# Optimization experiments

Hardware: AMD Instinct MI355X
Metric: run time of the kernel (lower is better)

The kernel has to match this reference:

```python
import jax, jax.numpy as jnp
import numpy as np

SEQ, BATCH, EMB, HID = 512, 256, 256, 512


def setup_inputs() -> dict:
    key = jax.random.key(0)
    ks = jax.random.split(key, 6)
    s_x = 1.0 / np.sqrt(EMB)
    s_h = 1.0 / np.sqrt(HID)
    return {
        "X": jax.random.normal(ks[0], (SEQ, BATCH, EMB), dtype=jnp.float32),
        # torch Linear weights are [out_features, in_features]
        "Wfx": jax.random.normal(ks[1], (HID, EMB), dtype=jnp.float32) * s_x,
        "Wix": jax.random.normal(ks[2], (HID, EMB), dtype=jnp.float32) * s_x,
        "Wox": jax.random.normal(ks[3], (HID, EMB), dtype=jnp.float32) * s_x,
        "Wax": jax.random.normal(ks[4], (HID, EMB), dtype=jnp.float32) * s_x,
        "Waa": jax.random.normal(ks[5], (HID, HID), dtype=jnp.float32) * s_h,
        # module initializes all biases to ones
        "bf": jnp.ones((HID,), dtype=jnp.float32),
        "bi": jnp.ones((HID,), dtype=jnp.float32),
        "bo": jnp.ones((HID,), dtype=jnp.float32),
        "ba": jnp.ones((HID,), dtype=jnp.float32),
    }


def reference(X, Wfx, Wix, Wox, Wax, Waa, bf, bi, bo, ba):
    # X: [seq, batch, emb]. Returns final hidden state h: [batch, hidden].
    batch = X.shape[1]
    hid = Waa.shape[0]

    def step(carry, x):
        h, c = carry
        ah = h @ Waa.T  # shared across all gates, as in the original
        # NOTE: original adds the bias twice (b + ... + b), kept faithfully
        ft = jax.nn.sigmoid(x @ Wfx.T + ah + 2.0 * bf)
        it = jax.nn.sigmoid(x @ Wix.T + ah + 2.0 * bi)
        ot = jax.nn.sigmoid(x @ Wox.T + ah + 2.0 * bo)
        cp = jnp.tanh(x @ Wax.T + ah + ba)
        c = ft * c + it * cp
        h = ot * jnp.tanh(c)
        return (h, c), None

    h0 = jnp.zeros((batch, hid), dtype=X.dtype)
    (h, _c), _ = jax.lax.scan(step, (h0, h0), X)
    return h
```

## Files before the change

### kernel.cpp

```cpp
#include <hip/hip_runtime.h>

#define SEQL 512
#define BATCH 256
#define EMB 256
#define HID 512
#define NTOT 2048

typedef __attribute__((ext_vector_type(8))) short bf16x8;
typedef __attribute__((ext_vector_type(4))) float f32x4;
typedef unsigned short u16;

static __device__ __forceinline__ u16 f2bf(float f) {
  unsigned u = __float_as_uint(f);
  u += 0x7FFFu + ((u >> 16) & 1u);
  return (u16)(u >> 16);
}
static __device__ __forceinline__ float bf2f(u16 s) {
  return __uint_as_float(((unsigned)s) << 16);
}
static __device__ __forceinline__ float sigmoidf_(float z) {
  return 1.f / (1.f + __expf(-z));
}
static __device__ __forceinline__ float tanhf_(float x) {
  float e = __expf(2.f * fabsf(x));
  float t = 1.f - 2.f / (e + 1.f);
  return copysignf(t, x);
}
static __device__ __forceinline__ f32x4 mfma16(bf16x8 a, bf16x8 b, f32x4 c) {
  return __builtin_amdgcn_mfma_f32_16x16x32_bf16(a, b, c, 0, 0, 0);
}
static __device__ __forceinline__ void gld16(const u16* g, u16* l) {
  __builtin_amdgcn_global_load_lds((const __attribute__((address_space(1))) void*)g,
                                   (__attribute__((address_space(3))) void*)l, 16, 0, 0);
}
static __device__ __forceinline__ bf16x8 ldx4_dev(const u16* p) {
  bf16x8 r;
  asm volatile("global_load_dwordx4 %0, %1, off sc1" : "=v"(r) : "v"(p));
  return r;
}
static __device__ __forceinline__ void st2_dev(u16* p, unsigned v) {
  asm volatile("global_store_short %0, %1, off sc1" :: "v"(p), "v"(v) : "memory");
}

__global__ void k_split(const float* __restrict__ src, u16* __restrict__ hi,
                        u16* __restrict__ lo, int n) {
  for (int i = blockIdx.x * blockDim.x + threadIdx.x; i < n;
       i += gridDim.x * blockDim.x) {
    float v = src[i];
    u16 h = f2bf(v);
    hi[i] = h;
    lo[i] = f2bf(v - bf2f(h));
  }
}

__global__ void k_bias2(const float* __restrict__ bf_, const float* __restrict__ bi_,
                        const float* __restrict__ bo_, const float* __restrict__ ba_,
                        float* __restrict__ bias2) {
  int n = blockIdx.x * blockDim.x + threadIdx.x;
  if (n >= NTOT) return;
  int g = n >> 9, j = n & 511;
  const float* p = (g == 0) ? bf_ : (g == 1) ? bi_ : (g == 2) ? bo_ : ba_;
  bias2[n] = ((g < 3) ? 2.f : 1.f) * p[j];
}

__global__ __launch_bounds__(256) void k_gemm(
    const u16* __restrict__ Ahi, const u16* __restrict__ Alo,
    const u16* __restrict__ Bhi, const u16* __restrict__ Blo,
    const float* __restrict__ bias2, float* __restrict__ G2) {
  __shared__ u16 lds[4][128 * 64];
  const int tid = threadIdx.x;
  const int lane = tid & 63;
  const int w = tid >> 6;
  const int wm = (w >> 1) * 64, wn = (w & 1) * 64;
  const int m0 = blockIdx.y * 128, n0 = blockIdx.x * 128;
  const int l15 = lane & 15, lhi = lane >> 4;

  f32x4 acc[4][4] = {};

  for (int k0 = 0; k0 < EMB; k0 += 64) {
    __syncthreads();
    for (int c = 0; c < 4; ++c) {
      int idx = tid + c * 256;
      int row = idx >> 3;
      int col = (idx & 7) * 8;
      long ga = (long)(m0 + row) * EMB + k0 + col;
      long gb = (long)(n0 + row) * EMB + k0 + col;
      gld16(Ahi + ga, &lds[0][idx * 8]);
      gld16(Alo + ga, &lds[1][idx * 8]);
      gld16(Bhi + gb, &lds[2][idx * 8]);
      gld16(Blo + gb, &lds[3][idx * 8]);
    }
    __syncthreads();
#pragma unroll
    for (int ks = 0; ks < 2; ++ks) {
      int ko = ks * 32 + lhi * 8;
      bf16x8 ah[4], al[4], bh[4], bl[4];
#pragma unroll
      for (int f = 0; f < 4; ++f) {
        int ra = (wm + f * 16 + l15) * 64 + ko;
        int rb = (wn + f * 16 + l15) * 64 + ko;
        ah[f] = *(const bf16x8*)&lds[0][ra];
        al[f] = *(const bf16x8*)&lds[1][ra];
        bh[f] = *(const bf16x8*)&lds[2][rb];
        bl[f] = *(const bf16x8*)&lds[3][rb];
      }
#pragma unroll
      for (int i = 0; i < 4; ++i)
#pragma unroll
        for (int j = 0; j < 4; ++j) {
          acc[i][j] = mfma16(ah[i], bh[j], acc[i][j]);
          acc[i][j] = mfma16(ah[i], bl[j], acc[i][j]);
          acc[i][j] = mfma16(al[i], bh[j], acc[i][j]);
        }
    }
  }
#pragma unroll
  for (int j = 0; j < 4; ++j) {
    int n = n0 + wn + j * 16 + l15;
    float bv = bias2[n];
    int g = n >> 9, jj = n & 511;
    int j16 = jj >> 4, j15 = jj & 15;
#pragma unroll
    for (int i = 0; i < 4; ++i) {
      int mb = m0 + wm + i * 16 + lhi * 4;
      int tloc = mb >> 8, brow = mb & 255;
      int bgrp = brow >> 4, bq = (brow >> 2) & 3;
      f32x4 v = acc[i][j];
      v[0] += bv; v[1] += bv; v[2] += bv; v[3] += bv;
      size_t addr = ((((size_t)(tloc * 16 + bgrp) * 32 + j16) * 4 + g) * 4 + bq) * 64 +
                    (size_t)j15 * 4;
      *(f32x4*)&G2[addr] = v;
    }
  }
}

__global__ __launch_bounds__(256, 1) void k_rnn(
    const u16* __restrict__ WaaHi, const u16* __restrict__ WaaLo,
    const float* __restrict__ G2,
    u16* __restrict__ h0hi, u16* __restrict__ h0lo,
    u16* __restrict__ h1hi, u16* __restrict__ h1lo,
    float* __restrict__ cSave, unsigned* __restrict__ flags,
    float* __restrict__ out, int t0, int nsteps) {
  const int tid = threadIdx.x;
  const int lane = tid & 63;
  const int w = tid >> 6;
  const int jsub = w >> 1, ksub = w & 1;
  const int l15 = lane & 15, lhi = lane >> 4;
  const int bid = blockIdx.x;
  const int grp = ((bid & 7) << 1) | ((bid >> 3) & 1);
  const int mem = bid >> 4;
  const int b0 = grp * 16;
  const int j0 = mem * 32 + jsub * 16;
  const int j16 = mem * 2 + jsub;
  const bool owner = (ksub == 0);

  __shared__ float red[2][64][4];

  bf16x8 wh[8], wl[8];
  {
    long base = (long)(j0 + l15) * HID + ksub * 256 + lhi * 8;
#pragma unroll
    for (int s = 0; s < 8; ++s) {
      wh[s] = *(const bf16x8*)&WaaHi[base + s * 32];
      wl[s] = *(const bf16x8*)&WaaLo[base + s * 32];
    }
#pragma unroll
    for (int s = 0; s < 8; ++s) {
      asm volatile("" : "+v"(wh[s]));
      asm volatile("" : "+v"(wl[s]));
    }
  }

  f32x4 c = {0.f, 0.f, 0.f, 0.f};
  const long cbase = (long)(b0 + lhi * 4) * HID + j0 + l15;
  if (owner && t0 > 0) {
#pragma unroll
    for (int r = 0; r < 4; ++r) c[r] = cSave[cbase + (long)r * HID];
  }

  const long abase = (long)(b0 + l15) * HID + ksub * 256 + lhi * 8;
  unsigned* flag = &flags[grp * 32];

  float gv[4][4];
  if (owner) {
    size_t tb = ((size_t)(0 * 16 + grp) * 32 + j16) * 1024;
#pragma unroll
    for (int g = 0; g < 4; ++g) {
      f32x4 v = *(const f32x4*)&G2[tb + (size_t)(g * 4 + lhi) * 64 + (size_t)l15 * 4];
#pragma unroll
      for (int r = 0; r < 4; ++r) gv[g][r] = v[r];
    }
  }

  for (int tl = 0; tl < nsteps; ++tl) {
    const int gt = t0 + tl;
    const u16* hHi = (gt & 1) ? h1hi : h0hi;
    const u16* hLo = (gt & 1) ? h1lo : h0lo;
    u16* nHi = (gt & 1) ? h0hi : h1hi;
    u16* nLo = (gt & 1) ? h0lo : h1lo;

    bf16x8 ah[8], al[8];
#pragma unroll
    for (int s = 0; s < 8; ++s) {
      ah[s] = ldx4_dev(hHi + abase + s * 32);
      al[s] = ldx4_dev(hLo + abase + s * 32);
    }
    asm volatile("s_waitcnt vmcnt(0)" ::: "memory");
    __builtin_amdgcn_sched_barrier(0);

    f32x4 a0 = {0.f, 0.f, 0.f, 0.f}, a1 = a0, a2 = a0;
#pragma unroll
    for (int s = 0; s < 8; ++s) {
      a0 = mfma16(ah[s], wh[s], a0);
      a1 = mfma16(ah[s], wl[s], a1);
      a2 = mfma16(al[s], wh[s], a2);
    }
    f32x4 acc = (a0 + a1) + a2;

    if (ksub == 1) *(f32x4*)&red[jsub][lane][0] = acc;

    float gvn[4][4];
    if (owner && tl + 1 < nsteps) {
      size_t tb = ((size_t)((tl + 1) * 16 + grp) * 32 + j16) * 1024;
#pragma unroll
      for (int g = 0; g < 4; ++g) {
        f32x4 v = *(const f32x4*)&G2[tb + (size_t)(g * 4 + lhi) * 64 + (size_t)l15 * 4];
#pragma unroll
        for (int r = 0; r < 4; ++r) gvn[g][r] = v[r];
      }
    }

    __syncthreads();
    if (owner) {
      f32x4 p = *(const f32x4*)&red[jsub][lane][0];
      acc += p;
#pragma unroll
      for (int r = 0; r < 4; ++r) {
        float z = acc[r];
        float ft = sigmoidf_(gv[0][r] + z);
        float it = sigmoidf_(gv[1][r] + z);
        float ot = sigmoidf_(gv[2][r] + z);
        float cp = tanhf_(gv[3][r] + z);
        c[r] = ft * c[r] + it * cp;
        float h = ot * tanhf_(c[r]);
        int b = b0 + lhi * 4 + r;
        int jj = j0 + l15;
        if (gt == SEQL - 1) {
          out[(long)b * HID + jj] = h;
        } else {
          u16 hh = f2bf(h);
          st2_dev(&nHi[(long)b * HID + jj], (unsigned)hh);
          st2_dev(&nLo[(long)b * HID + jj], (unsigned)f2bf(h - bf2f(hh)));
        }
      }
      if (tl + 1 < nsteps) {
#pragma unroll
        for (int g = 0; g < 4; ++g)
#pragma unroll
          for (int r = 0; r < 4; ++r) gv[g][r] = gvn[g][r];
      }
    }

    if (tl + 1 < nsteps) {
      asm volatile("s_waitcnt vmcnt(0)" ::: "memory");
      if ((tid & 127) == 0) {
        unsigned one = 1u;
        asm volatile("global_atomic_add %0, %1, off sc1" :: "v"(flag), "v"(one)
                     : "memory");
      }
      if (tid == 0) {
        unsigned tgt = 32u * (unsigned)(tl + 1);
        long guard = 0;
        unsigned v;
        for (;;) {
          asm volatile("global_load_dword %0, %1, off sc0 sc1\n\ts_waitcnt vmcnt(0)"
                       : "=v"(v) : "v"(flag) : "memory");
          if (v >= tgt) break;
          __builtin_amdgcn_s_sleep(1);
          if (++guard > (1L << 22)) break;
        }
      }
      __syncthreads();
    }
  }

  if (owner && t0 + nsteps < SEQL) {
#pragma unroll
    for (int r = 0; r < 4; ++r) cSave[cbase + (long)r * HID] = c[r];
  }
}

extern "C" void kernel_launch(void* const* d_in, const int* in_sizes, int n_in,
                              void* d_out, int out_size, void* d_ws, size_t ws_size,
                              hipStream_t stream) {
  const float* X   = (const float*)d_in[0];
  const float* Wfx = (const float*)d_in[1];
  const float* Wix = (const float*)d_in[2];
  const float* Wox = (const float*)d_in[3];
  const float* Wax = (const float*)d_in[4];
  const float* Waa = (const float*)d_in[5];
  const float* bfp = (const float*)d_in[6];
  const float* bip = (const float*)d_in[7];
  const float* bop = (const float*)d_in[8];
  const float* bap = (const float*)d_in[9];
  float* out = (float*)d_out;

  char* ws = (char*)d_ws;
  size_t off = 0;
  auto take = [&](size_t n) {
    void* p = ws + off;
    off += (n + 255) & ~(size_t)255;
    return p;
  };
  u16* WxHi  = (u16*)take((size_t)NTOT * EMB * 2);
  u16* WxLo  = (u16*)take((size_t)NTOT * EMB * 2);
  u16* WaaHi = (u16*)take((size_t)HID * HID * 2);
  u16* WaaLo = (u16*)take((size_t)HID * HID * 2);
  float* bias2 = (float*)take((size_t)NTOT * 4);
  u16* h0hi = (u16*)take((size_t)BATCH * HID * 2);
  u16* h0lo = (u16*)take((size_t)BATCH * HID * 2);
  u16* h1hi = (u16*)take((size_t)BATCH * HID * 2);
  u16* h1lo = (u16*)take((size_t)BATCH * HID * 2);
  float* cSave = (float*)take((size_t)BATCH * HID * 4);
  unsigned* flags = (unsigned*)take(16 * 32 * 4);
  size_t fixed_end = off;

  const size_t perstep = (size_t)BATCH * EMB * 2 * 2 + (size_t)BATCH * NTOT * 4;
  int C = 0;
  const int cands[] = {512, 256, 128, 64, 32, 16, 8, 4, 2, 1};
  for (int cand : cands)
    if (fixed_end + (size_t)cand * perstep <= ws_size) { C = cand; break; }
  if (C == 0) return;

  u16* XcHi = (u16*)take((size_t)C * BATCH * EMB * 2);
  u16* XcLo = (u16*)take((size_t)C * BATCH * EMB * 2);
  float* G2 = (float*)take((size_t)C * BATCH * NTOT * 4);

  const float* wx[4] = {Wfx, Wix, Wox, Wax};
  for (int g = 0; g < 4; ++g)
    k_split<<<256, 256, 0, stream>>>(wx[g], WxHi + (size_t)g * HID * EMB,
                                     WxLo + (size_t)g * HID * EMB, HID * EMB);
  k_split<<<512, 256, 0, stream>>>(Waa, WaaHi, WaaLo, HID * HID);
  k_bias2<<<8, 256, 0, stream>>>(bfp, bip, bop, bap, bias2);
  hipMemsetAsync(h0hi, 0, (size_t)BATCH * HID * 2 * 2, stream);

  const int nch = SEQL / C;
  for (int ch = 0; ch < nch; ++ch) {
    int t0 = ch * C;
    hipMemsetAsync(flags, 0, 16 * 32 * 4, stream);
    k_split<<<2048, 256, 0, stream>>>(X + (size_t)t0 * BATCH * EMB, XcHi, XcLo,
                                      C * BATCH * EMB);
    dim3 gg(NTOT / 128, C * 2);
    k_gemm<<<gg, 256, 0, stream>>>(XcHi, XcLo, WxHi, WxLo, bias2, G2);
    k_rnn<<<256, 256, 0, stream>>>(WaaHi, WaaLo, G2, h0hi, h0lo, h1hi, h1lo,
                                   cSave, flags, out, t0, C);
  }
}
```

Measured before the change: 3.807 ms.

## Restructure recurrent kernel to 64 blocks with LDS-resident weights and fused X split

The recurrent kernel now runs on 64 blocks instead of 256, and each block owns 128 hidden units. Waa is pre-packed into MFMA fragment order: the hi half stays in registers and the lo half is staged in LDS. The aim is fewer blocks taking part in each per-step cross-block barrier, and larger per-wave work. The X hi/lo split is fused into the input GEMM's LDS staging, which removes a separate split kernel and its buffers. The G2 layout is changed to match the new tiling. The trade-off is that per-step compute per block grows about fourfold and runs on only 64 CUs, so the serial step latency could rise.

After: 4.966 ms. 1.3x slower.

```diff
diff --git a/kernel.cpp b/kernel.cpp
--- a/kernel.cpp
+++ b/kernel.cpp
@@ -8,6 +8,7 @@
 
 typedef __attribute__((ext_vector_type(8))) short bf16x8;
 typedef __attribute__((ext_vector_type(4))) float f32x4;
+typedef __attribute__((ext_vector_type(4))) unsigned short us4;
 typedef unsigned short u16;
 
 static __device__ __forceinline__ u16 f2bf(float f) {
@@ -40,6 +41,16 @@
 }
 static __device__ __forceinline__ void st2_dev(u16* p, unsigned v) {
   asm volatile("global_store_short %0, %1, off sc1" :: "v"(p), "v"(v) : "memory");
+}
+static __device__ __forceinline__ void flag_add_dev(unsigned* p) {
+  unsigned one = 1u;
+  asm volatile("global_atomic_add %0, %1, off sc1" :: "v"(p), "v"(one) : "memory");
+}
+static __device__ __forceinline__ unsigned flag_poll_dev(const unsigned* p) {
+  unsigned v;
+  asm volatile("global_load_dword %0, %1, off sc0 sc1\ns_waitcnt vmcnt(0)"
+               : "=v"(v) : "v"(p) : "memory");
+  return v;
 }
 
 __global__ void k_split(const float* __restrict__ src, u16* __restrict__ hi,
@@ -63,8 +74,27 @@
   bias2[n] = ((g < 3) ? 2.f : 1.f) * p[j];
 }
 
+__global__ void k_packW(const float* __restrict__ Waa, u16* __restrict__ WPhi,
+                        u16* __restrict__ WPlo) {
+  int idx = blockIdx.x * 256 + threadIdx.x;
+  int lane = idx & 63;
+  int fi = idx >> 6;
+  if (fi >= 512) return;
+  int kf = fi & 7, nf = (fi >> 3) & 3, w = (fi >> 5) & 3, mem = fi >> 7;
+  int j = mem * 128 + (w >> 1) * 64 + nf * 16 + (lane & 15);
+  int k0 = (w & 1) * 256 + kf * 32 + (lane >> 4) * 8;
+  size_t base = (size_t)idx * 8;
+#pragma unroll
+  for (int e = 0; e < 8; ++e) {
+    float v = Waa[(size_t)j * HID + k0 + e];
+    u16 h = f2bf(v);
+    WPhi[base + e] = h;
+    WPlo[base + e] = f2bf(v - bf2f(h));
+  }
+}
+
 __global__ __launch_bounds__(256) void k_gemm(
-    const u16* __restrict__ Ahi, const u16* __restrict__ Alo,
+    const float* __restrict__ X,
     const u16* __restrict__ Bhi, const u16* __restrict__ Blo,
     const float* __restrict__ bias2, float* __restrict__ G2) {
   __shared__ u16 lds[4][128 * 64];
@@ -79,16 +109,30 @@
 
   for (int k0 = 0; k0 < EMB; k0 += 64) {
     __syncthreads();
+#pragma unroll
     for (int c = 0; c < 4; ++c) {
       int idx = tid + c * 256;
       int row = idx >> 3;
       int col = (idx & 7) * 8;
-      long ga = (long)(m0 + row) * EMB + k0 + col;
-      long gb = (long)(n0 + row) * EMB + k0 + col;
-      gld16(Ahi + ga, &lds[0][idx * 8]);
-      gld16(Alo + ga, &lds[1][idx * 8]);
+      size_t gb = (size_t)(n0 + row) * EMB + k0 + col;
       gld16(Bhi + gb, &lds[2][idx * 8]);
       gld16(Blo + gb, &lds[3][idx * 8]);
+    }
+#pragma unroll
+    for (int c = 0; c < 8; ++c) {
+      int idx = tid + c * 256;
+      int row = idx >> 4;
+      int c4 = (idx & 15) * 4;
+      f32x4 xv = *(const f32x4*)&X[(size_t)(m0 + row) * EMB + k0 + c4];
+      us4 h4, l4;
+#pragma unroll
+      for (int e = 0; e < 4; ++e) {
+        u16 h = f2bf(xv[e]);
+        h4[e] = h;
+        l4[e] = f2bf(xv[e] - bf2f(h));
+      }
+      *(us4*)&lds[0][row * 64 + c4] = h4;
+      *(us4*)&lds[1][row * 64 + c4] = l4;
     }
     __syncthreads();
 #pragma unroll
@@ -119,174 +163,161 @@
     int n = n0 + wn + j * 16 + l15;
     float bv = bias2[n];
     int g = n >> 9, jj = n & 511;
-    int j16 = jj >> 4, j15 = jj & 15;
 #pragma unroll
     for (int i = 0; i < 4; ++i) {
       int mb = m0 + wm + i * 16 + lhi * 4;
       int tloc = mb >> 8, brow = mb & 255;
-      int bgrp = brow >> 4, bq = (brow >> 2) & 3;
+      int bgrp = brow >> 4, b15 = brow & 15;
       f32x4 v = acc[i][j];
       v[0] += bv; v[1] += bv; v[2] += bv; v[3] += bv;
-      size_t addr = ((((size_t)(tloc * 16 + bgrp) * 32 + j16) * 4 + g) * 4 + bq) * 64 +
-                    (size_t)j15 * 4;
+      size_t addr = ((((size_t)tloc * 16 + bgrp) * 4 + g) * 512 + jj) * 16 + b15;
       *(f32x4*)&G2[addr] = v;
     }
   }
 }
 
 __global__ __launch_bounds__(256, 1) void k_rnn(
-    const u16* __restrict__ WaaHi, const u16* __restrict__ WaaLo,
+    const u16* __restrict__ WPhi, const u16* __restrict__ WPlo,
     const float* __restrict__ G2,
-    u16* __restrict__ h0hi, u16* __restrict__ h0lo,
-    u16* __restrict__ h1hi, u16* __restrict__ h1lo,
+    u16* __restrict__ hAhi, u16* __restrict__ hAlo,
+    u16* __restrict__ hBhi, u16* __restrict__ hBlo,
     float* __restrict__ cSave, unsigned* __restrict__ flags,
     float* __restrict__ out, int t0, int nsteps) {
+  extern __shared__ u16 smem[];
   const int tid = threadIdx.x;
   const int lane = tid & 63;
   const int w = tid >> 6;
-  const int jsub = w >> 1, ksub = w & 1;
   const int l15 = lane & 15, lhi = lane >> 4;
   const int bid = blockIdx.x;
-  const int grp = ((bid & 7) << 1) | ((bid >> 3) & 1);
+  const int grp = bid & 15;
   const int mem = bid >> 4;
+  const int jsub = w >> 1, ksub = w & 1;
+  const bool owner = (ksub == 0);
   const int b0 = grp * 16;
-  const int j0 = mem * 32 + jsub * 16;
-  const int j16 = mem * 2 + jsub;
-  const bool owner = (ksub == 0);
-
-  __shared__ float red[2][64][4];
-
-  bf16x8 wh[8], wl[8];
+  const int j0 = mem * 128 + jsub * 64;
+  char* smB = (char*)smem;
+
+  bf16x8 BH[4][8];
   {
-    long base = (long)(j0 + l15) * HID + ksub * 256 + lhi * 8;
-#pragma unroll
-    for (int s = 0; s < 8; ++s) {
-      wh[s] = *(const bf16x8*)&WaaHi[base + s * 32];
-      wl[s] = *(const bf16x8*)&WaaLo[base + s * 32];
-    }
-#pragma unroll
-    for (int s = 0; s < 8; ++s) {
-      asm volatile("" : "+v"(wh[s]));
-      asm volatile("" : "+v"(wl[s]));
-    }
-  }
-
-  f32x4 c = {0.f, 0.f, 0.f, 0.f};
-  const long cbase = (long)(b0 + lhi * 4) * HID + j0 + l15;
+    size_t fb = ((size_t)mem * 4 + w) * 32;
+#pragma unroll
+    for (int q = 0; q < 32; ++q)
+      gld16(WPlo + (fb + q) * 512 + lane * 8,
+            smem + ((size_t)w * 32 + q) * 512 + lane * 8);
+#pragma unroll
+    for (int nf = 0; nf < 4; ++nf)
+#pragma unroll
+      for (int kf = 0; kf < 8; ++kf) {
+        BH[nf][kf] = *(const bf16x8*)(WPhi + (fb + nf * 8 + kf) * 512 + lane * 8);
+        asm volatile("" : "+v"(BH[nf][kf]));
+      }
+  }
+
+  f32x4 cc[4] = {};
+  const size_t ctbase = ((size_t)bid * 256 + tid) * 16;
   if (owner && t0 > 0) {
 #pragma unroll
-    for (int r = 0; r < 4; ++r) c[r] = cSave[cbase + (long)r * HID];
-  }
-
-  const long abase = (long)(b0 + l15) * HID + ksub * 256 + lhi * 8;
-  unsigned* flag = &flags[grp * 32];
-
-  float gv[4][4];
-  if (owner) {
-    size_t tb = ((size_t)(0 * 16 + grp) * 32 + j16) * 1024;
-#pragma unroll
-    for (int g = 0; g < 4; ++g) {
-      f32x4 v = *(const f32x4*)&G2[tb + (size_t)(g * 4 + lhi) * 64 + (size_t)l15 * 4];
-#pragma unroll
-      for (int r = 0; r < 4; ++r) gv[g][r] = v[r];
-    }
-  }
+    for (int nf = 0; nf < 4; ++nf) cc[nf] = *(const f32x4*)&cSave[ctbase + nf * 4];
+  }
+
+  const size_t abase = (size_t)(b0 + l15) * HID + ksub * 256 + lhi * 8;
+  unsigned* stepflag = flags + grp * 32;
+  __syncthreads();
 
   for (int tl = 0; tl < nsteps; ++tl) {
     const int gt = t0 + tl;
-    const u16* hHi = (gt & 1) ? h1hi : h0hi;
-    const u16* hLo = (gt & 1) ? h1lo : h0lo;
-    u16* nHi = (gt & 1) ? h0hi : h1hi;
-    u16* nLo = (gt & 1) ? h0lo : h1lo;
-
-    bf16x8 ah[8], al[8];
-#pragma unroll
-    for (int s = 0; s < 8; ++s) {
-      ah[s] = ldx4_dev(hHi + abase + s * 32);
-      al[s] = ldx4_dev(hLo + abase + s * 32);
-    }
-    asm volatile("s_waitcnt vmcnt(0)" ::: "memory");
-    __builtin_amdgcn_sched_barrier(0);
-
-    f32x4 a0 = {0.f, 0.f, 0.f, 0.f}, a1 = a0, a2 = a0;
-#pragma unroll
-    for (int s = 0; s < 8; ++s) {
-      a0 = mfma16(ah[s], wh[s], a0);
-      a1 = mfma16(ah[s], wl[s], a1);
-      a2 = mfma16(al[s], wh[s], a2);
-    }
-    f32x4 acc = (a0 + a1) + a2;
-
-    if (ksub == 1) *(f32x4*)&red[jsub][lane][0] = acc;
-
-    float gvn[4][4];
-    if (owner && tl + 1 < nsteps) {
-      size_t tb = ((size_t)((tl + 1) * 16 + grp) * 32 + j16) * 1024;
-#pragma unroll
-      for (int g = 0; g < 4; ++g) {
-        f32x4 v = *(const f32x4*)&G2[tb + (size_t)(g * 4 + lhi) * 64 + (size_t)l15 * 4];
-#pragma unroll
-        for (int r = 0; r < 4; ++r) gvn[g][r] = v[r];
-      }
-    }
-
-    __syncthreads();
+    const u16* hHi = (gt & 1) ? hBhi : hAhi;
+    const u16* hLo = (gt & 1) ? hBlo : hAlo;
+    u16* nHi = (gt & 1) ? hAhi : hBhi;
+    u16* nLo = (gt & 1) ? hAlo : hBlo;
+
+    f32x4 gq[4][4];
     if (owner) {
-      f32x4 p = *(const f32x4*)&red[jsub][lane][0];
-      acc += p;
-#pragma unroll
-      for (int r = 0; r < 4; ++r) {
-        float z = acc[r];
-        float ft = sigmoidf_(gv[0][r] + z);
-        float it = sigmoidf_(gv[1][r] + z);
-        float ot = sigmoidf_(gv[2][r] + z);
-        float cp = tanhf_(gv[3][r] + z);
-        c[r] = ft * c[r] + it * cp;
-        float h = ot * tanhf_(c[r]);
-        int b = b0 + lhi * 4 + r;
-        int jj = j0 + l15;
-        if (gt == SEQL - 1) {
-          out[(long)b * HID + jj] = h;
-        } else {
-          u16 hh = f2bf(h);
-          st2_dev(&nHi[(long)b * HID + jj], (unsigned)hh);
-          st2_dev(&nLo[(long)b * HID + jj], (unsigned)f2bf(h - bf2f(hh)));
-        }
-      }
-      if (tl + 1 < nsteps) {
+      const float* gp = G2 + ((size_t)tl * 16 + grp) * 4 * 512 * 16;
+#pragma unroll
+      for (int nf = 0; nf < 4; ++nf)
 #pragma unroll
         for (int g = 0; g < 4; ++g)
-#pragma unroll
-          for (int r = 0; r < 4; ++r) gv[g][r] = gvn[g][r];
-      }
-    }
-
-    if (tl + 1 < nsteps) {
-      asm volatile("s_waitcnt vmcnt(0)" ::: "memory");
-      if ((tid & 127) == 0) {
-        unsigned one = 1u;
-        asm volatile("global_atomic_add %0, %1, off sc1" :: "v"(flag), "v"(one)
-                     : "memory");
-      }
+          gq[nf][g] = *(const f32x4*)(gp + ((size_t)g * 512 + j0 + nf * 16 + l15) * 16 + lhi * 4);
+    }
+
+    if (tl > 0) {
       if (tid == 0) {
-        unsigned tgt = 32u * (unsigned)(tl + 1);
+        unsigned tgt = 8u * (unsigned)tl;
         long guard = 0;
-        unsigned v;
-        for (;;) {
-          asm volatile("global_load_dword %0, %1, off sc0 sc1\n\ts_waitcnt vmcnt(0)"
-                       : "=v"(v) : "v"(flag) : "memory");
-          if (v >= tgt) break;
+        while (flag_poll_dev(stepflag) < tgt) {
           __builtin_amdgcn_s_sleep(1);
           if (++guard > (1L << 22)) break;
         }
       }
       __syncthreads();
     }
+
+    bf16x8 aH[8], aL[8];
+#pragma unroll
+    for (int kf = 0; kf < 8; ++kf) {
+      aH[kf] = ldx4_dev(hHi + abase + kf * 32);
+      aL[kf] = ldx4_dev(hLo + abase + kf * 32);
+    }
+    asm volatile("s_waitcnt vmcnt(0)" ::: "memory");
+    __builtin_amdgcn_sched_barrier(0);
+
+    f32x4 acc[4];
+#pragma unroll
+    for (int nf = 0; nf < 4; ++nf) {
+      f32x4 p0 = {0.f, 0.f, 0.f, 0.f}, p1 = p0, p2 = p0;
+#pragma unroll
+      for (int kf = 0; kf < 8; ++kf) {
+        bf16x8 bl = *(const bf16x8*)(smB + ((size_t)(w * 32 + nf * 8 + kf)) * 1024 + lane * 16);
+        p0 = mfma16(aH[kf], BH[nf][kf], p0);
+        p1 = mfma16(aL[kf], BH[nf][kf], p1);
+        p2 = mfma16(aH[kf], bl, p2);
+      }
+      acc[nf] = (p0 + p1) + p2;
+    }
+
+    if (!owner) {
+#pragma unroll
+      for (int nf = 0; nf < 4; ++nf)
+        *(f32x4*)(smB + 131072 + ((size_t)(jsub * 4 + nf) * 64 + lane) * 16) = acc[nf];
+    }
+    __syncthreads();
+
+    if (owner) {
+#pragma unroll
+      for (int nf = 0; nf < 4; ++nf) {
+        acc[nf] += *(const f32x4*)(smB + 131072 + ((size_t)(jsub * 4 + nf) * 64 + lane) * 16);
+#pragma unroll
+        for (int r = 0; r < 4; ++r) {
+          float z = acc[nf][r];
+          float ft = sigmoidf_(gq[nf][0][r] + z);
+          float it = sigmoidf_(gq[nf][1][r] + z);
+          float ot = sigmoidf_(gq[nf][2][r] + z);
+          float cp = tanhf_(gq[nf][3][r] + z);
+          float cn = ft * cc[nf][r] + it * cp;
+          cc[nf][r] = cn;
+          float h = ot * tanhf_(cn);
+          int b = b0 + lhi * 4 + r;
+          int j = j0 + nf * 16 + l15;
+          if (gt == SEQL - 1) {
+            out[(size_t)b * HID + j] = h;
+          } else {
+            u16 hh = f2bf(h), hl = f2bf(h - bf2f(hh));
+            st2_dev(nHi + (size_t)b * HID + j, (unsigned)hh);
+            st2_dev(nLo + (size_t)b * HID + j, (unsigned)hl);
+          }
+        }
+      }
+      if (gt != SEQL - 1) {
+        asm volatile("s_waitcnt vmcnt(0)" ::: "memory");
+        if (lane == 0) flag_add_dev(stepflag);
+      }
+    }
   }
 
   if (owner && t0 + nsteps < SEQL) {
 #pragma unroll
-    for (int r = 0; r < 4; ++r) cSave[cbase + (long)r * HID] = c[r];
+    for (int nf = 0; nf < 4; ++nf) *(f32x4*)&cSave[ctbase + nf * 4] = cc[nf];
   }
 }
 
@@ -312,47 +343,46 @@
     off += (n + 255) & ~(size_t)255;
     return p;
   };
-  u16* WxHi  = (u16*)take((size_t)NTOT * EMB * 2);
-  u16* WxLo  = (u16*)take((size_t)NTOT * EMB * 2);
-  u16* WaaHi = (u16*)take((size_t)HID * HID * 2);
-  u16* WaaLo = (u16*)take((size_t)HID * HID * 2);
+  u16* WxHi   = (u16*)take((size_t)NTOT * EMB * 2);
+  u16* WxLo   = (u16*)take((size_t)NTOT * EMB * 2);
+  u16* WPhi   = (u16*)take((size_t)512 * 512 * 2);
+  u16* WPlo   = (u16*)take((size_t)512 * 512 * 2);
   float* bias2 = (float*)take((size_t)NTOT * 4);
-  u16* h0hi = (u16*)take((size_t)BATCH * HID * 2);
-  u16* h0lo = (u16*)take((size_t)BATCH * HID * 2);
-  u16* h1hi = (u16*)take((size_t)BATCH * HID * 2);
-  u16* h1lo = (u16*)take((size_t)BATCH * HID * 2);
-  float* cSave = (float*)take((size_t)BATCH * HID * 4);
+  u16* hAhi = (u16*)take((size_t)BATCH * HID * 2);
+  u16* hAlo = (u16*)take((size_t)BATCH * HID * 2);
+  u16* hBhi = (u16*)take((size_t)BATCH * HID * 2);
+  u16* hBlo = (u16*)take((size_t)BATCH * HID * 2);
+  float* cSave = (float*)take((size_t)64 * 256 * 16 * 4);
   unsigned* flags = (unsigned*)take(16 * 32 * 4);
   size_t fixed_end = off;
 
-  const size_t perstep = (size_t)BATCH * EMB * 2 * 2 + (size_t)BATCH * NTOT * 4;
+  const size_t perstep = (size_t)BATCH * NTOT * 4;
   int C = 0;
   const int cands[] = {512, 256, 128, 64, 32, 16, 8, 4, 2, 1};
   for (int cand : cands)
     if (fixed_end + (size_t)cand * perstep <= ws_size) { C = cand; break; }
   if (C == 0) return;
-
-  u16* XcHi = (u16*)take((size_t)C * BATCH * EMB * 2);
-  u16* XcLo = (u16*)take((size_t)C * BATCH * EMB * 2);
-  float* G2 = (float*)take((size_t)C * BATCH * NTOT * 4);
+  float* G2 = (float*)take((size_t)C * perstep);
+
+  (void)hipFuncSetAttribute((const void*)k_rnn,
+                            hipFuncAttributeMaxDynamicSharedMemorySize, 139264);
 
   const float* wx[4] = {Wfx, Wix, Wox, Wax};
   for (int g = 0; g < 4; ++g)
     k_split<<<256, 256, 0, stream>>>(wx[g], WxHi + (size_t)g * HID * EMB,
                                      WxLo + (size_t)g * HID * EMB, HID * EMB);
-  k_split<<<512, 256, 0, stream>>>(Waa, WaaHi, WaaLo, HID * HID);
+  k_packW<<<128, 256, 0, stream>>>(Waa, WPhi, WPlo);
   k_bias2<<<8, 256, 0, stream>>>(bfp, bip, bop, bap, bias2);
-  hipMemsetAsync(h0hi, 0, (size_t)BATCH * HID * 2 * 2, stream);
+  hipMemsetAsync(hAhi, 0, (size_t)BATCH * HID * 2 * 2, stream);
 
   const int nch = SEQL / C;
   for (int ch = 0; ch < nch; ++ch) {
     int t0 = ch * C;
     hipMemsetAsync(flags, 0, 16 * 32 * 4, stream);
-    k_split<<<2048, 256, 0, stream>>>(X + (size_t)t0 * BATCH * EMB, XcHi, XcLo,
-                                      C * BATCH * EMB);
     dim3 gg(NTOT / 128, C * 2);
-    k_gemm<<<gg, 256, 0, stream>>>(XcHi, XcLo, WxHi, WxLo, bias2, G2);
-    k_rnn<<<256, 256, 0, stream>>>(WaaHi, WaaLo, G2, h0hi, h0lo, h1hi, h1lo,
-                                   cSave, flags, out, t0, C);
-  }
-}
+    k_gemm<<<gg, 256, 0, stream>>>(X + (size_t)t0 * BATCH * EMB, WxHi, WxLo,
+                                   bias2, G2);
+    k_rnn<<<64, 256, 139264, stream>>>(WPhi, WPlo, G2, hAhi, hAlo, hBhi, hBlo,
+                                       cSave, flags, out, t0, C);
+  }
+}
```
